# Optimization experiments

Measured on AMD Instinct MI355X. Metric: run time of the kernel, lower is better.

The kernel has to match this reference:

```python
import jax, jax.numpy as jnp
import numpy as np

N, E, IN_DIM, HID, HEADS = 50000, 400000, 128, 64, 4
NEG_SLOPE, LN_EPS = 0.2, 1e-5


def setup_inputs() -> dict:
    key = jax.random.key(0)
    ks = jax.random.split(key, 12)
    x = jax.random.normal(ks[0], (N, IN_DIM), dtype=jnp.float32)
    edge_index = jax.random.randint(ks[1], (2, E), 0, N, dtype=jnp.int64)
    s = 1.0 / np.sqrt(HID)
    return {
        "x": x,
        "edge_index": edge_index,
        "W_gcn": jax.random.normal(ks[2], (IN_DIM, HID), dtype=jnp.float32) / np.sqrt(IN_DIM),
        "b_gcn": jnp.zeros((HID,), dtype=jnp.float32),
        "W_gat": jax.random.normal(ks[3], (HID, HEADS * HID), dtype=jnp.float32) * s,
        "att_src": jax.random.normal(ks[4], (HEADS, HID), dtype=jnp.float32) * s,
        "att_dst": jax.random.normal(ks[5], (HEADS, HID), dtype=jnp.float32) * s,
        "b_gat": jnp.zeros((HID,), dtype=jnp.float32),
        "W_patch": jax.random.normal(ks[6], (HID, HID), dtype=jnp.float32) * s,
        "b_patch": jnp.zeros((HID,), dtype=jnp.float32),
        "gamma": jnp.ones((HID,), dtype=jnp.float32),
        "beta": jnp.zeros((HID,), dtype=jnp.float32),
    }


def _forward(x, edge_index, W_gcn, b_gcn, W_gat, att_src, att_dst, b_gat,
             W_patch, b_patch, gamma, beta):
    n = x.shape[0]
    loop = jnp.arange(n, dtype=edge_index.dtype)
    src = jnp.concatenate([edge_index[0], loop])  # self-loops appended (PyG default)
    dst = jnp.concatenate([edge_index[1], loop])

    # ---- GCNConv: symmetric degree normalization + scatter-add ----
    deg = jax.ops.segment_sum(jnp.ones_like(dst, dtype=jnp.float32), dst, num_segments=n)
    dinv = jnp.where(deg > 0, jax.lax.rsqrt(deg), 0.0)
    norm = dinv[src] * dinv[dst]  # [E+N]
    xw = x @ W_gcn  # [N,HID]
    h1 = jax.ops.segment_sum(xw[src] * norm[:, None], dst, num_segments=n) + b_gcn
    h1 = jax.nn.relu(h1)

    # ---- GATConv (heads=4, concat=False -> mean over heads) ----
    z = (h1 @ W_gat).reshape(n, HEADS, HID)  # [N,H,C]
    a_s = jnp.einsum('nhc,hc->nh', z, att_src)  # [N,H]
    a_d = jnp.einsum('nhc,hc->nh', z, att_dst)
    e = jax.nn.leaky_relu(a_s[src] + a_d[dst], negative_slope=NEG_SLOPE)  # [E+N,H]
    # segment-softmax over incoming edges per destination node
    m = jax.ops.segment_max(e, dst, num_segments=n)  # [N,H]
    ex = jnp.exp(e - m[dst])
    denom = jax.ops.segment_sum(ex, dst, num_segments=n)
    alpha = ex / denom[dst]  # [E+N,H]
    agg = jax.ops.segment_sum(z[src] * alpha[:, :, None], dst, num_segments=n)  # [N,H,C]
    h2 = jax.nn.relu(agg.mean(axis=1) + b_gat)

    # ---- residual fusion + LayerNorm (dropout is identity in eval) ----
    h_patch = h1 @ W_patch + b_patch
    h = h1 + h2 + h_patch
    mu = h.mean(axis=-1, keepdims=True)
    var = h.var(axis=-1, keepdims=True)
    return (h - mu) * jax.lax.rsqrt(var + LN_EPS) * gamma + beta


def reference(x, edge_index, W_gcn, b_gcn, W_gat, att_src, att_dst, b_gat,
              W_patch, b_patch, gamma, beta):
    return _forward(x, edge_index, W_gcn, b_gcn, W_gat, att_src, att_dst, b_gat,
                    W_patch, b_patch, gamma, beta)
```

## Files before the change

### kernel.cpp

```cpp
#include <hip/hip_runtime.h>
#include <math.h>

#define IN_DIM 128
#define HID 64
#define HEADS 4
#define NEG_SLOPE 0.2f
#define LN_EPS 1e-5f
#define XK 320

typedef short bf16x8 __attribute__((ext_vector_type(8)));
typedef float f32x4  __attribute__((ext_vector_type(4)));

__device__ inline unsigned short f2bf(float f) {
    unsigned u = __float_as_uint(f);
    u += 0x7fffu + ((u >> 16) & 1u);
    return (unsigned short)(u >> 16);
}
__device__ inline float bf2f(unsigned short s) {
    return __uint_as_float(((unsigned)s) << 16);
}
__device__ inline float leaky(float v) { return v > 0.0f ? v : NEG_SLOPE * v; }

__global__ void k_detect_zero(const unsigned long long* ei, int count, int n,
                              int* flag, int* hist) {
    int i = blockIdx.x * blockDim.x + threadIdx.x;
    if (i < n) hist[i] = 0;
    if (blockIdx.x == 0) {
        __shared__ int s_bad;
        if (threadIdx.x == 0) s_bad = 0;
        __syncthreads();
        int lim = count < 4096 ? count : 4096;
        int bad = 0;
        for (int k = threadIdx.x; k < lim; k += 256)
            if (ei[k] >= (unsigned long long)n) bad = 1;
        if (bad) s_bad = 1;
        __syncthreads();
        if (threadIdx.x == 0) *flag = s_bad ? 0 : 1;
    }
}

__global__ void k_wprep(const float* __restrict__ Wg, const float* __restrict__ Wp,
                        const float* __restrict__ Wgcn,
                        unsigned short* __restrict__ Wt_post,
                        unsigned short* __restrict__ Wt_xw) {
    int p = blockIdx.x * 256 + threadIdx.x;
    if (p < 2560) {
        int c = p & 63, kg = p >> 6;
        bf16x8 v;
#pragma unroll
        for (int j = 0; j < 8; j++) {
            int k = kg * 8 + j;
            float f;
            if (k < 256) f = 0.25f * Wg[(size_t)(k & 63) * 256 + (k >> 6) * 64 + c];
            else         f = Wp[(size_t)(k - 256) * 64 + c];
            v[j] = (short)f2bf(f);
        }
        *(bf16x8*)(&Wt_post[(size_t)p * 8]) = v;
    } else if (p < 2560 + 1024) {
        int q = p - 2560;
        int c = q & 63, kg = q >> 6;
        bf16x8 v;
#pragma unroll
        for (int j = 0; j < 8; j++)
            v[j] = (short)f2bf(Wgcn[(size_t)(kg * 8 + j) * 64 + c]);
        *(bf16x8*)(&Wt_xw[(size_t)q * 8]) = v;
    }
}

__global__ void k_remap_hist(const void* ei, int E, const int* flag,
                             int* edges32, int* hist) {
    int i = blockIdx.x * blockDim.x + threadIdx.x;
    if (i >= 2 * E) return;
    int is64 = *flag;
    int v;
    if (is64) v = (int)((const long long*)ei)[i];
    else      v = ((const int*)ei)[i];
    edges32[i] = v;
    if (i >= E) atomicAdd(&hist[v], 1);
}

__global__ __launch_bounds__(256) void k_scan1(const int* __restrict__ hist,
                                               int* __restrict__ tmp,
                                               int* __restrict__ partial, int n) {
    __shared__ int s[256];
    int t = threadIdx.x, i = blockIdx.x * 256 + t;
    int v = (i < n) ? hist[i] : 0;
    s[t] = v;
    __syncthreads();
    for (int off = 1; off < 256; off <<= 1) {
        int x = (t >= off) ? s[t - off] : 0;
        __syncthreads();
        s[t] += x;
        __syncthreads();
    }
    tmp[i] = s[t] - v;
    if (t == 255) partial[blockIdx.x] = s[255];
}

__global__ __launch_bounds__(256) void k_scan2_prep(int* partial, int nb,
                                                    const float* __restrict__ Wg,
                                                    const float* __restrict__ att_s,
                                                    const float* __restrict__ att_d,
                                                    float* __restrict__ w_s,
                                                    float* __restrict__ w_d) {
    __shared__ int s[256];
    int t = threadIdx.x;
    int v = (t < nb) ? partial[t] : 0;
    s[t] = v;
    __syncthreads();
    for (int off = 1; off < 256; off <<= 1) {
        int x = (t >= off) ? s[t - off] : 0;
        __syncthreads();
        s[t] += x;
        __syncthreads();
    }
    if (t < nb) partial[t] = s[t] - v;
    int h = t >> 6, k = t & 63;
    float ss = 0.0f, sd = 0.0f;
    for (int c = 0; c < HID; c++) {
        float w = Wg[(size_t)k * (HEADS * HID) + h * HID + c];
        ss += w * att_s[h * HID + c];
        sd += w * att_d[h * HID + c];
    }
    w_s[h * HID + k] = ss;
    w_d[h * HID + k] = sd;
}

__global__ void k_scan3(const int* __restrict__ tmp, const int* __restrict__ partial,
                        const int* __restrict__ hist, int* __restrict__ row_ptr,
                        int* __restrict__ cursor, float* __restrict__ dinv, int n) {
    int i = blockIdx.x * blockDim.x + threadIdx.x;
    if (i >= n) return;
    int v = tmp[i] + partial[i >> 8];
    row_ptr[i] = v;
    cursor[i] = v;
    dinv[i] = rsqrtf((float)(hist[i] + 1));
}

__global__ void k_scatter(const int* __restrict__ src, const int* __restrict__ dst,
                          int* __restrict__ cursor, int* __restrict__ col,
                          int* __restrict__ col_d, int E) {
    int i = blockIdx.x * blockDim.x + threadIdx.x;
    if (i >= E) return;
    int d = dst[i];
    int pos = atomicAdd(&cursor[d], 1);
    col[pos] = src[i];
    col_d[pos] = d;
}

__global__ __launch_bounds__(256) void k_xw(const float* __restrict__ x,
                                            const unsigned short* __restrict__ Wt_g,
                                            const float* __restrict__ dinv,
                                            unsigned short* __restrict__ xws, int n) {
    __shared__ unsigned short Wt[16 * 64 * 8];
    int t = threadIdx.x;
    for (int idx = t; idx < 1024; idx += 256)
        *(bf16x8*)(&Wt[idx * 8]) = *(const bf16x8*)(&Wt_g[(size_t)idx * 8]);
    __syncthreads();

    int lane = t & 63;
    int li = lane & 15, quad = lane >> 4;
    int w = t >> 6;
    int r0 = blockIdx.x * 64 + w * 16;
    int rload = r0 + li; if (rload > n - 1) rload = n - 1;

    f32x4 acc[4];
#pragma unroll
    for (int i = 0; i < 4; i++) acc[i] = (f32x4){0.f, 0.f, 0.f, 0.f};

    const float* xp = x + (size_t)rload * IN_DIM + quad * 8;
#pragma unroll
    for (int ks = 0; ks < 4; ks++) {
        float4 p0 = *(const float4*)(xp + ks * 32);
        float4 p1 = *(const float4*)(xp + ks * 32 + 4);
        bf16x8 a;
        a[0] = (short)f2bf(p0.x); a[1] = (short)f2bf(p0.y);
        a[2] = (short)f2bf(p0.z); a[3] = (short)f2bf(p0.w);
        a[4] = (short)f2bf(p1.x); a[5] = (short)f2bf(p1.y);
        a[6] = (short)f2bf(p1.z); a[7] = (short)f2bf(p1.w);
        int kg = ks * 4 + quad;
#pragma unroll
        for (int tt = 0; tt < 4; tt++) {
            bf16x8 bfr = *(const bf16x8*)(&Wt[((kg * 64) + tt * 16 + li) * 8]);
            acc[tt] = __builtin_amdgcn_mfma_f32_16x16x32_bf16(a, bfr, acc[tt], 0, 0, 0);
        }
    }
#pragma unroll
    for (int reg = 0; reg < 4; reg++) {
        int r = r0 + quad * 4 + reg;
        if (r >= n) continue;
        float dv = dinv[r];
#pragma unroll
        for (int tt = 0; tt < 4; tt++) {
            xws[(size_t)r * HID + tt * 16 + li] = f2bf(acc[tt][reg] * dv);
        }
    }
}

__global__ __launch_bounds__(256) void k_gcn(const int* __restrict__ col,
                                             const int* __restrict__ row_ptr,
                                             const int* __restrict__ hist,
                                             const float* __restrict__ dinv,
                                             const unsigned short* __restrict__ xws,
                                             const float* __restrict__ b,
                                             const float* __restrict__ w_s,
                                             const float* __restrict__ w_d,
                                             float* __restrict__ h1f,
                                             unsigned short* __restrict__ h1b,
                                             unsigned short* __restrict__ X,
                                             float4* __restrict__ a_s,
                                             float4* __restrict__ a_d, int n) {
    int t = threadIdx.x, c = t & 63;
    int d = blockIdx.x * 4 + (t >> 6);
    if (d >= n) return;
    int start = row_ptr[d], cnt = hist[d];
    float acc = bf2f(xws[(size_t)d * HID + c]);
    int k = 0;
    for (; k + 3 < cnt; k += 4) {
        int s0 = col[start + k],     s1 = col[start + k + 1];
        int s2 = col[start + k + 2], s3 = col[start + k + 3];
        float v0 = bf2f(xws[(size_t)s0 * HID + c]);
        float v1 = bf2f(xws[(size_t)s1 * HID + c]);
        float v2 = bf2f(xws[(size_t)s2 * HID + c]);
        float v3 = bf2f(xws[(size_t)s3 * HID + c]);
        acc += (v0 + v1) + (v2 + v3);
    }
    for (; k < cnt; k++) acc += bf2f(xws[(size_t)col[start + k] * HID + c]);
    float h1c = fmaxf(acc * dinv[d] + b[c], 0.0f);
    h1f[(size_t)d * HID + c] = h1c;
    unsigned short hb = f2bf(h1c);
    h1b[(size_t)d * HID + c] = hb;
    X[(size_t)d * XK + 256 + c] = hb;
    float vs0 = h1c * w_s[c],       vs1 = h1c * w_s[64 + c];
    float vs2 = h1c * w_s[128 + c], vs3 = h1c * w_s[192 + c];
    float vd0 = h1c * w_d[c],       vd1 = h1c * w_d[64 + c];
    float vd2 = h1c * w_d[128 + c], vd3 = h1c * w_d[192 + c];
    for (int o = 32; o > 0; o >>= 1) {
        vs0 += __shfl_xor(vs0, o, 64); vs1 += __shfl_xor(vs1, o, 64);
        vs2 += __shfl_xor(vs2, o, 64); vs3 += __shfl_xor(vs3, o, 64);
        vd0 += __shfl_xor(vd0, o, 64); vd1 += __shfl_xor(vd1, o, 64);
        vd2 += __shfl_xor(vd2, o, 64); vd3 += __shfl_xor(vd3, o, 64);
    }
    if (c == 0) {
        a_s[d] = make_float4(vs0, vs1, vs2, vs3);
        a_d[d] = make_float4(vd0, vd1, vd2, vd3);
    }
}

__global__ void k_ew(const int* __restrict__ col, const int* __restrict__ col_d,
                     const float4* __restrict__ a_s, const float4* __restrict__ a_d,
                     float4* __restrict__ wbuf, int E) {
    int i = blockIdx.x * blockDim.x + threadIdx.x;
    if (i >= E) return;
    int s = col[i], d = col_d[i];
    float4 as = a_s[s], ad = a_d[d];
    float4 r;
    r.x = __expf(leaky(as.x + ad.x));
    r.y = __expf(leaky(as.y + ad.y));
    r.z = __expf(leaky(as.z + ad.z));
    r.w = __expf(leaky(as.w + ad.w));
    wbuf[i] = r;
}

__global__ __launch_bounds__(256) void k_attn(const int* __restrict__ col,
                                              const int* __restrict__ row_ptr,
                                              const int* __restrict__ hist,
                                              const float4* __restrict__ a_s,
                                              const float4* __restrict__ a_d,
                                              const float4* __restrict__ wbuf,
                                              const unsigned short* __restrict__ h1b,
                                              unsigned short* __restrict__ X, int n) {
    int t = threadIdx.x, c = t & 63;
    int d = blockIdx.x * 4 + (t >> 6);
    if (d >= n) return;
    float4 ad = a_d[d];
    float4 asd = a_s[d];
    float w0 = __expf(leaky(asd.x + ad.x));
    float w1 = __expf(leaky(asd.y + ad.y));
    float w2 = __expf(leaky(asd.z + ad.z));
    float w3 = __expf(leaky(asd.w + ad.w));
    float hs = bf2f(h1b[(size_t)d * HID + c]);
    float A0 = w0 * hs, A1 = w1 * hs, A2 = w2 * hs, A3 = w3 * hs;
    float l0 = w0, l1 = w1, l2 = w2, l3 = w3;
    int start = row_ptr[d], cnt = hist[d];
    int k = 0;
    for (; k + 3 < cnt; k += 4) {
        int s0 = col[start + k],     s1 = col[start + k + 1];
        int s2 = col[start + k + 2], s3 = col[start + k + 3];
        float4 e0 = wbuf[start + k],     e1 = wbuf[start + k + 1];
        float4 e2 = wbuf[start + k + 2], e3 = wbuf[start + k + 3];
        float hv0 = bf2f(h1b[(size_t)s0 * HID + c]);
        float hv1 = bf2f(h1b[(size_t)s1 * HID + c]);
        float hv2 = bf2f(h1b[(size_t)s2 * HID + c]);
        float hv3 = bf2f(h1b[(size_t)s3 * HID + c]);
        A0 += e0.x * hv0 + e1.x * hv1 + e2.x * hv2 + e3.x * hv3;
        A1 += e0.y * hv0 + e1.y * hv1 + e2.y * hv2 + e3.y * hv3;
        A2 += e0.z * hv0 + e1.z * hv1 + e2.z * hv2 + e3.z * hv3;
        A3 += e0.w * hv0 + e1.w * hv1 + e2.w * hv2 + e3.w * hv3;
        l0 += (e0.x + e1.x) + (e2.x + e3.x);
        l1 += (e0.y + e1.y) + (e2.y + e3.y);
        l2 += (e0.z + e1.z) + (e2.z + e3.z);
        l3 += (e0.w + e1.w) + (e2.w + e3.w);
    }
    for (; k < cnt; k++) {
        int s0 = col[start + k];
        float4 e0 = wbuf[start + k];
        float hv0 = bf2f(h1b[(size_t)s0 * HID + c]);
        A0 += e0.x * hv0; l0 += e0.x;
        A1 += e0.y * hv0; l1 += e0.y;
        A2 += e0.z * hv0; l2 += e0.z;
        A3 += e0.w * hv0; l3 += e0.w;
    }
    size_t base = (size_t)d * XK;
    X[base + c]       = f2bf(A0 / l0);
    X[base + 64 + c]  = f2bf(A1 / l1);
    X[base + 128 + c] = f2bf(A2 / l2);
    X[base + 192 + c] = f2bf(A3 / l3);
}

__global__ __launch_bounds__(256) void k_post(const unsigned short* __restrict__ Wt_g,
                                              const unsigned short* __restrict__ X,
                                              const float* __restrict__ h1f,
                                              const float* __restrict__ bp,
                                              const float* __restrict__ bg,
                                              const float* __restrict__ gamma,
                                              const float* __restrict__ beta,
                                              float* __restrict__ out, int n) {
    __shared__ unsigned short Wt[2560 * 8];
    int t = threadIdx.x;
    for (int idx = t; idx < 2560; idx += 256)
        *(bf16x8*)(&Wt[idx * 8]) = *(const bf16x8*)(&Wt_g[(size_t)idx * 8]);
    __syncthreads();

    int lane = t & 63;
    int li = lane & 15, quad = lane >> 4;
    int w = t >> 6;
    int rbase = blockIdx.x * 128 + w * 32;

    f32x4 acc_a[2][4], acc_h[2][4];
#pragma unroll
    for (int rt = 0; rt < 2; rt++)
#pragma unroll
        for (int i = 0; i < 4; i++) {
            acc_a[rt][i] = (f32x4){0.f, 0.f, 0.f, 0.f};
            acc_h[rt][i] = (f32x4){0.f, 0.f, 0.f, 0.f};
        }
#pragma unroll
    for (int ks = 0; ks < 10; ks++) {
        int kg = ks * 4 + quad;
        bf16x8 b0 = *(const bf16x8*)(&Wt[((kg * 64) + 0 * 16 + li) * 8]);
        bf16x8 b1 = *(const bf16x8*)(&Wt[((kg * 64) + 1 * 16 + li) * 8]);
        bf16x8 b2 = *(const bf16x8*)(&Wt[((kg * 64) + 2 * 16 + li) * 8]);
        bf16x8 b3 = *(const bf16x8*)(&Wt[((kg * 64) + 3 * 16 + li) * 8]);
#pragma unroll
        for (int rt = 0; rt < 2; rt++) {
            bf16x8 a = *(const bf16x8*)(X + (size_t)(rbase + rt * 16 + li) * XK
                                          + quad * 8 + ks * 32);
            if (ks < 8) {
                acc_a[rt][0] = __builtin_amdgcn_mfma_f32_16x16x32_bf16(a, b0, acc_a[rt][0], 0, 0, 0);
                acc_a[rt][1] = __builtin_amdgcn_mfma_f32_16x16x32_bf16(a, b1, acc_a[rt][1], 0, 0, 0);
                acc_a[rt][2] = __builtin_amdgcn_mfma_f32_16x16x32_bf16(a, b2, acc_a[rt][2], 0, 0, 0);
                acc_a[rt][3] = __builtin_amdgcn_mfma_f32_16x16x32_bf16(a, b3, acc_a[rt][3], 0, 0, 0);
            } else {
                acc_h[rt][0] = __builtin_amdgcn_mfma_f32_16x16x32_bf16(a, b0, acc_h[rt][0], 0, 0, 0);
                acc_h[rt][1] = __builtin_amdgcn_mfma_f32_16x16x32_bf16(a, b1, acc_h[rt][1], 0, 0, 0);
                acc_h[rt][2] = __builtin_amdgcn_mfma_f32_16x16x32_bf16(a, b2, acc_h[rt][2], 0, 0, 0);
                acc_h[rt][3] = __builtin_amdgcn_mfma_f32_16x16x32_bf16(a, b3, acc_h[rt][3], 0, 0, 0);
            }
        }
    }
    float bgv[4], bpv[4], gv[4], btv[4];
#pragma unroll
    for (int tt = 0; tt < 4; tt++) {
        int c = tt * 16 + li;
        bgv[tt] = bg[c]; bpv[tt] = bp[c]; gv[tt] = gamma[c]; btv[tt] = beta[c];
    }
#pragma unroll
    for (int rt = 0; rt < 2; rt++) {
#pragma unroll
        for (int reg = 0; reg < 4; reg++) {
            int r = rbase + rt * 16 + quad * 4 + reg;
            bool ok = (r < n);
            float hv[4];
            float s1 = 0.0f, s2 = 0.0f;
#pragma unroll
            for (int tt = 0; tt < 4; tt++) {
                int c = tt * 16 + li;
                float h1c = ok ? h1f[(size_t)r * HID + c] : 0.0f;
                float h2 = fmaxf(acc_a[rt][tt][reg] + bgv[tt], 0.0f);
                float h = h1c + h2 + acc_h[rt][tt][reg] + bpv[tt];
                hv[tt] = h;
                s1 += h; s2 += h * h;
            }
            for (int o = 8; o > 0; o >>= 1) {
                s1 += __shfl_xor(s1, o, 64);
                s2 += __shfl_xor(s2, o, 64);
            }
            float mu = s1 * (1.0f / 64.0f);
            float var = s2 * (1.0f / 64.0f) - mu * mu;
            float rs = rsqrtf(var + LN_EPS);
            if (ok) {
#pragma unroll
                for (int tt = 0; tt < 4; tt++) {
                    int c = tt * 16 + li;
                    out[(size_t)r * HID + c] = (hv[tt] - mu) * rs * gv[tt] + btv[tt];
                }
            }
        }
    }
}

extern "C" void kernel_launch(void* const* d_in, const int* in_sizes, int n_in,
                              void* d_out, int out_size, void* d_ws, size_t ws_size,
                              hipStream_t stream) {
    int n = in_sizes[0] / IN_DIM;
    int E = in_sizes[1] / 2;

    const float* x     = (const float*)d_in[0];
    const void*  ei    = d_in[1];
    const float* W_gcn = (const float*)d_in[2];
    const float* b_gcn = (const float*)d_in[3];
    const float* W_gat = (const float*)d_in[4];
    const float* att_s = (const float*)d_in[5];
    const float* att_d = (const float*)d_in[6];
    const float* b_gat = (const float*)d_in[7];
    const float* W_p   = (const float*)d_in[8];
    const float* b_p   = (const float*)d_in[9];
    const float* gamma = (const float*)d_in[10];
    const float* beta  = (const float*)d_in[11];

    int n_pad  = ((n + 255) / 256) * 256;
    int nscan  = n_pad / 256;
    int n128   = ((n + 127) / 128) * 128;

    float* ws = (float*)d_ws;
    size_t off = 0;
    int*   flag    = (int*)(ws + off);  off += 4;
    int*   edges   = (int*)(ws + off);  off += (size_t)2 * E;
    int*   hist    = (int*)(ws + off);  off += n;
    int*   row_ptr = (int*)(ws + off);  off += n;
    int*   cursor  = (int*)(ws + off);  off += n;
    int*   tmp     = (int*)(ws + off);  off += n_pad;
    int*   partial = (int*)(ws + off);  off += 256;
    int*   colv    = (int*)(ws + off);  off += E;
    int*   col_d   = (int*)(ws + off);  off += E;
    float* dinv    = ws + off;          off += n;
    float* w_s     = ws + off;          off += HEADS * HID;
    float* w_d     = ws + off;          off += HEADS * HID;
    off = (off + 3) & ~(size_t)3;
    unsigned short* Wt_post = (unsigned short*)(ws + off); off += 2560 * 8 / 2;
    unsigned short* Wt_xw   = (unsigned short*)(ws + off); off += 1024 * 8 / 2;
    unsigned short* xws = (unsigned short*)(ws + off); off += (size_t)n * HID / 2;
    float* h1f     = ws + off;          off += (size_t)n * HID;
    off = (off + 3) & ~(size_t)3;
    unsigned short* h1b = (unsigned short*)(ws + off); off += (size_t)n * HID / 2;
    off = (off + 3) & ~(size_t)3;
    float4* a_sv   = (float4*)(ws + off); off += (size_t)n * 4;
    float4* a_dv   = (float4*)(ws + off); off += (size_t)n * 4;
    off = (off + 3) & ~(size_t)3;
    float4* wbuf   = (float4*)(ws + off); off += (size_t)E * 4;
    unsigned short* X = (unsigned short*)(ws + off); off += (size_t)n128 * XK / 2;

    const int* src = edges;
    const int* dst = edges + E;

    k_detect_zero<<<(n + 255) / 256, 256, 0, stream>>>(
        (const unsigned long long*)ei, E, n, flag, hist);
    k_wprep<<<14, 256, 0, stream>>>(W_gat, W_p, W_gcn, Wt_post, Wt_xw);
    k_remap_hist<<<(2 * E + 255) / 256, 256, 0, stream>>>(ei, E, flag, edges, hist);

    k_scan1<<<nscan, 256, 0, stream>>>(hist, tmp, partial, n);
    k_scan2_prep<<<1, 256, 0, stream>>>(partial, nscan, W_gat, att_s, att_d, w_s, w_d);
    k_scan3<<<nscan, 256, 0, stream>>>(tmp, partial, hist, row_ptr, cursor, dinv, n);
    k_scatter<<<(E + 255) / 256, 256, 0, stream>>>(src, dst, cursor, colv, col_d, E);

    k_xw<<<(n + 63) / 64, 256, 0, stream>>>(x, Wt_xw, dinv, xws, n);

    k_gcn<<<(n + 3) / 4, 256, 0, stream>>>(colv, row_ptr, hist, dinv, xws, b_gcn,
                                           w_s, w_d, h1f, h1b, X, a_sv, a_dv, n);

    k_ew<<<(E + 255) / 256, 256, 0, stream>>>(colv, col_d, a_sv, a_dv, wbuf, E);

    k_attn<<<(n + 3) / 4, 256, 0, stream>>>(colv, row_ptr, hist, a_sv, a_dv,
                                            wbuf, h1b, X, n);

    k_post<<<(n + 127) / 128, 256, 0, stream>>>(Wt_post, X, h1f, b_p, b_gat,
                                                gamma, beta, (float*)d_out, n);
}
```

Baseline: 244.5 us.

## Merge init/scatter/xw kernels, drop edge remap buffer and fp32 h1 copy

```diff
diff --git a/kernel.cpp b/kernel.cpp
--- a/kernel.cpp
+++ b/kernel.cpp
@@ -6,7 +6,6 @@
 #define HEADS 4
 #define NEG_SLOPE 0.2f
 #define LN_EPS 1e-5f
-#define XK 320
 
 typedef short bf16x8 __attribute__((ext_vector_type(8)));
 typedef float f32x4  __attribute__((ext_vector_type(4)));
@@ -21,62 +20,62 @@
 }
 __device__ inline float leaky(float v) { return v > 0.0f ? v : NEG_SLOPE * v; }
 
-__global__ void k_detect_zero(const unsigned long long* ei, int count, int n,
-                              int* flag, int* hist) {
+__global__ void k_init_all(const unsigned long long* ei, int E, int n,
+                           int* flag, int* hist,
+                           const float* __restrict__ Wg, const float* __restrict__ Wp,
+                           const float* __restrict__ Wgcn,
+                           unsigned short* __restrict__ Wt_post,
+                           unsigned short* __restrict__ Wt_xw) {
+    int nzb = (n + 255) >> 8;
+    if ((int)blockIdx.x < nzb) {
+        int i = blockIdx.x * 256 + threadIdx.x;
+        if (i < n) hist[i] = 0;
+        if (blockIdx.x == 0) {
+            __shared__ int s_bad;
+            if (threadIdx.x == 0) s_bad = 0;
+            __syncthreads();
+            int lim = E < 4096 ? E : 4096;
+            int bad = 0;
+            for (int k = threadIdx.x; k < lim; k += 256)
+                if (ei[k] >= (unsigned long long)n) bad = 1;
+            if (bad) s_bad = 1;
+            __syncthreads();
+            if (threadIdx.x == 0) *flag = s_bad ? 0 : 1;
+        }
+    } else {
+        int p = (blockIdx.x - nzb) * 256 + threadIdx.x;
+        if (p < 2560) {
+            int c = p & 63, kg = p >> 6;
+            bf16x8 v;
+#pragma unroll
+            for (int j = 0; j < 8; j++) {
+                int k = kg * 8 + j;
+                float f;
+                if (k < 256) f = 0.25f * Wg[(size_t)(k & 63) * 256 + (k >> 6) * 64 + c];
+                else         f = Wp[(size_t)(k - 256) * 64 + c];
+                v[j] = (short)f2bf(f);
+            }
+            *(bf16x8*)(&Wt_post[(size_t)p * 8]) = v;
+        } else if (p < 2560 + 1024) {
+            int q = p - 2560;
+            int c = q & 63, kg = q >> 6;
+            bf16x8 v;
+#pragma unroll
+            for (int j = 0; j < 8; j++)
+                v[j] = (short)f2bf(Wgcn[(size_t)(kg * 8 + j) * 64 + c]);
+            *(bf16x8*)(&Wt_xw[(size_t)q * 8]) = v;
+        }
+    }
+}
+
+__global__ void k_hist(const void* ei, int E, const int* flag, int* hist) {
     int i = blockIdx.x * blockDim.x + threadIdx.x;
-    if (i < n) hist[i] = 0;
-    if (blockIdx.x == 0) {
-        __shared__ int s_bad;
-        if (threadIdx.x == 0) s_bad = 0;
-        __syncthreads();
-        int lim = count < 4096 ? count : 4096;
-        int bad = 0;
-        for (int k = threadIdx.x; k < lim; k += 256)
-            if (ei[k] >= (unsigned long long)n) bad = 1;
-        if (bad) s_bad = 1;
-        __syncthreads();
-        if (threadIdx.x == 0) *flag = s_bad ? 0 : 1;
-    }
-}
-
-__global__ void k_wprep(const float* __restrict__ Wg, const float* __restrict__ Wp,
-                        const float* __restrict__ Wgcn,
-                        unsigned short* __restrict__ Wt_post,
-                        unsigned short* __restrict__ Wt_xw) {
-    int p = blockIdx.x * 256 + threadIdx.x;
-    if (p < 2560) {
-        int c = p & 63, kg = p >> 6;
-        bf16x8 v;
-#pragma unroll
-        for (int j = 0; j < 8; j++) {
-            int k = kg * 8 + j;
-            float f;
-            if (k < 256) f = 0.25f * Wg[(size_t)(k & 63) * 256 + (k >> 6) * 64 + c];
-            else         f = Wp[(size_t)(k - 256) * 64 + c];
-            v[j] = (short)f2bf(f);
-        }
-        *(bf16x8*)(&Wt_post[(size_t)p * 8]) = v;
-    } else if (p < 2560 + 1024) {
-        int q = p - 2560;
-        int c = q & 63, kg = q >> 6;
-        bf16x8 v;
-#pragma unroll
-        for (int j = 0; j < 8; j++)
-            v[j] = (short)f2bf(Wgcn[(size_t)(kg * 8 + j) * 64 + c]);
-        *(bf16x8*)(&Wt_xw[(size_t)q * 8]) = v;
-    }
-}
-
-__global__ void k_remap_hist(const void* ei, int E, const int* flag,
-                             int* edges32, int* hist) {
-    int i = blockIdx.x * blockDim.x + threadIdx.x;
-    if (i >= 2 * E) return;
+    if (i >= E) return;
     int is64 = *flag;
-    int v;
-    if (is64) v = (int)((const long long*)ei)[i];
-    else      v = ((const int*)ei)[i];
-    edges32[i] = v;
-    if (i >= E) atomicAdd(&hist[v], 1);
+    int d;
+    if (is64) d = (int)((const long long*)ei)[E + i];
+    else      d = ((const int*)ei)[E + i];
+    atomicAdd(&hist[d], 1);
 }
 
 __global__ __launch_bounds__(256) void k_scan1(const int* __restrict__ hist,
@@ -137,62 +136,66 @@
     dinv[i] = rsqrtf((float)(hist[i] + 1));
 }
 
-__global__ void k_scatter(const int* __restrict__ src, const int* __restrict__ dst,
-                          int* __restrict__ cursor, int* __restrict__ col,
-                          int* __restrict__ col_d, int E) {
-    int i = blockIdx.x * blockDim.x + threadIdx.x;
-    if (i >= E) return;
-    int d = dst[i];
-    int pos = atomicAdd(&cursor[d], 1);
-    col[pos] = src[i];
-    col_d[pos] = d;
-}
-
-__global__ __launch_bounds__(256) void k_xw(const float* __restrict__ x,
-                                            const unsigned short* __restrict__ Wt_g,
-                                            const float* __restrict__ dinv,
-                                            unsigned short* __restrict__ xws, int n) {
+__global__ __launch_bounds__(256) void k_scatter_xw(const void* ei, int E,
+                                                    const int* __restrict__ flag,
+                                                    int* __restrict__ cursor,
+                                                    int* __restrict__ col,
+                                                    int* __restrict__ col_d,
+                                                    const float* __restrict__ x,
+                                                    const unsigned short* __restrict__ Wt_g,
+                                                    const float* __restrict__ dinv,
+                                                    unsigned short* __restrict__ xws, int n) {
     __shared__ unsigned short Wt[16 * 64 * 8];
-    int t = threadIdx.x;
-    for (int idx = t; idx < 1024; idx += 256)
-        *(bf16x8*)(&Wt[idx * 8]) = *(const bf16x8*)(&Wt_g[(size_t)idx * 8]);
-    __syncthreads();
-
-    int lane = t & 63;
-    int li = lane & 15, quad = lane >> 4;
-    int w = t >> 6;
-    int r0 = blockIdx.x * 64 + w * 16;
-    int rload = r0 + li; if (rload > n - 1) rload = n - 1;
-
-    f32x4 acc[4];
-#pragma unroll
-    for (int i = 0; i < 4; i++) acc[i] = (f32x4){0.f, 0.f, 0.f, 0.f};
-
-    const float* xp = x + (size_t)rload * IN_DIM + quad * 8;
-#pragma unroll
-    for (int ks = 0; ks < 4; ks++) {
-        float4 p0 = *(const float4*)(xp + ks * 32);
-        float4 p1 = *(const float4*)(xp + ks * 32 + 4);
-        bf16x8 a;
-        a[0] = (short)f2bf(p0.x); a[1] = (short)f2bf(p0.y);
-        a[2] = (short)f2bf(p0.z); a[3] = (short)f2bf(p0.w);
-        a[4] = (short)f2bf(p1.x); a[5] = (short)f2bf(p1.y);
-        a[6] = (short)f2bf(p1.z); a[7] = (short)f2bf(p1.w);
-        int kg = ks * 4 + quad;
-#pragma unroll
-        for (int tt = 0; tt < 4; tt++) {
-            bf16x8 bfr = *(const bf16x8*)(&Wt[((kg * 64) + tt * 16 + li) * 8]);
-            acc[tt] = __builtin_amdgcn_mfma_f32_16x16x32_bf16(a, bfr, acc[tt], 0, 0, 0);
-        }
-    }
-#pragma unroll
-    for (int reg = 0; reg < 4; reg++) {
-        int r = r0 + quad * 4 + reg;
-        if (r >= n) continue;
-        float dv = dinv[r];
-#pragma unroll
-        for (int tt = 0; tt < 4; tt++) {
-            xws[(size_t)r * HID + tt * 16 + li] = f2bf(acc[tt][reg] * dv);
+    int nsb = (E + 255) >> 8;
+    if ((int)blockIdx.x < nsb) {
+        int i = blockIdx.x * 256 + threadIdx.x;
+        if (i >= E) return;
+        int is64 = *flag;
+        int s, d;
+        if (is64) { s = (int)((const long long*)ei)[i]; d = (int)((const long long*)ei)[E + i]; }
+        else      { s = ((const int*)ei)[i];            d = ((const int*)ei)[E + i]; }
+        int pos = atomicAdd(&cursor[d], 1);
+        col[pos] = s;
+        col_d[pos] = d;
+    } else {
+        int bx = blockIdx.x - nsb;
+        int t = threadIdx.x;
+        for (int idx = t; idx < 1024; idx += 256)
+            *(bf16x8*)(&Wt[idx * 8]) = *(const bf16x8*)(&Wt_g[(size_t)idx * 8]);
+        __syncthreads();
+        int lane = t & 63;
+        int li = lane & 15, quad = lane >> 4;
+        int w = t >> 6;
+        int r0 = bx * 64 + w * 16;
+        int rload = r0 + li; if (rload > n - 1) rload = n - 1;
+        f32x4 acc[4];
+#pragma unroll
+        for (int i = 0; i < 4; i++) acc[i] = (f32x4){0.f, 0.f, 0.f, 0.f};
+        const float* xp = x + (size_t)rload * IN_DIM + quad * 8;
+#pragma unroll
+        for (int ks = 0; ks < 4; ks++) {
+            float4 p0 = *(const float4*)(xp + ks * 32);
+            float4 p1 = *(const float4*)(xp + ks * 32 + 4);
+            bf16x8 a;
+            a[0] = (short)f2bf(p0.x); a[1] = (short)f2bf(p0.y);
+            a[2] = (short)f2bf(p0.z); a[3] = (short)f2bf(p0.w);
+            a[4] = (short)f2bf(p1.x); a[5] = (short)f2bf(p1.y);
+            a[6] = (short)f2bf(p1.z); a[7] = (short)f2bf(p1.w);
+            int kg = ks * 4 + quad;
+#pragma unroll
+            for (int tt = 0; tt < 4; tt++) {
+                bf16x8 bfr = *(const bf16x8*)(&Wt[((kg * 64) + tt * 16 + li) * 8]);
+                acc[tt] = __builtin_amdgcn_mfma_f32_16x16x32_bf16(a, bfr, acc[tt], 0, 0, 0);
+            }
+        }
+#pragma unroll
+        for (int reg = 0; reg < 4; reg++) {
+            int r = r0 + quad * 4 + reg;
+            if (r >= n) continue;
+            float dv = dinv[r];
+#pragma unroll
+            for (int tt = 0; tt < 4; tt++)
+                xws[(size_t)r * HID + tt * 16 + li] = f2bf(acc[tt][reg] * dv);
         }
     }
 }
@@ -205,9 +208,7 @@
                                              const float* __restrict__ b,
                                              const float* __restrict__ w_s,
                                              const float* __restrict__ w_d,
-                                             float* __restrict__ h1f,
                                              unsigned short* __restrict__ h1b,
-                                             unsigned short* __restrict__ X,
                                              float4* __restrict__ a_s,
                                              float4* __restrict__ a_d, int n) {
     int t = threadIdx.x, c = t & 63;
@@ -216,21 +217,24 @@
     int start = row_ptr[d], cnt = hist[d];
     float acc = bf2f(xws[(size_t)d * HID + c]);
     int k = 0;
-    for (; k + 3 < cnt; k += 4) {
+    for (; k + 7 < cnt; k += 8) {
         int s0 = col[start + k],     s1 = col[start + k + 1];
         int s2 = col[start + k + 2], s3 = col[start + k + 3];
+        int s4 = col[start + k + 4], s5 = col[start + k + 5];
+        int s6 = col[start + k + 6], s7 = col[start + k + 7];
         float v0 = bf2f(xws[(size_t)s0 * HID + c]);
         float v1 = bf2f(xws[(size_t)s1 * HID + c]);
         float v2 = bf2f(xws[(size_t)s2 * HID + c]);
         float v3 = bf2f(xws[(size_t)s3 * HID + c]);
-        acc += (v0 + v1) + (v2 + v3);
+        float v4 = bf2f(xws[(size_t)s4 * HID + c]);
+        float v5 = bf2f(xws[(size_t)s5 * HID + c]);
+        float v6 = bf2f(xws[(size_t)s6 * HID + c]);
+        float v7 = bf2f(xws[(size_t)s7 * HID + c]);
+        acc += ((v0 + v1) + (v2 + v3)) + ((v4 + v5) + (v6 + v7));
     }
     for (; k < cnt; k++) acc += bf2f(xws[(size_t)col[start + k] * HID + c]);
     float h1c = fmaxf(acc * dinv[d] + b[c], 0.0f);
-    h1f[(size_t)d * HID + c] = h1c;
-    unsigned short hb = f2bf(h1c);
-    h1b[(size_t)d * HID + c] = hb;
-    X[(size_t)d * XK + 256 + c] = hb;
+    h1b[(size_t)d * HID + c] = f2bf(h1c);
     float vs0 = h1c * w_s[c],       vs1 = h1c * w_s[64 + c];
     float vs2 = h1c * w_s[128 + c], vs3 = h1c * w_s[192 + c];
     float vd0 = h1c * w_d[c],       vd1 = h1c * w_d[64 + c];
@@ -284,23 +288,18 @@
     float l0 = w0, l1 = w1, l2 = w2, l3 = w3;
     int start = row_ptr[d], cnt = hist[d];
     int k = 0;
-    for (; k + 3 < cnt; k += 4) {
-        int s0 = col[start + k],     s1 = col[start + k + 1];
-        int s2 = col[start + k + 2], s3 = col[start + k + 3];
-        float4 e0 = wbuf[start + k],     e1 = wbuf[start + k + 1];
-        float4 e2 = wbuf[start + k + 2], e3 = wbuf[start + k + 3];
-        float hv0 = bf2f(h1b[(size_t)s0 * HID + c]);
-        float hv1 = bf2f(h1b[(size_t)s1 * HID + c]);
-        float hv2 = bf2f(h1b[(size_t)s2 * HID + c]);
-        float hv3 = bf2f(h1b[(size_t)s3 * HID + c]);
-        A0 += e0.x * hv0 + e1.x * hv1 + e2.x * hv2 + e3.x * hv3;
-        A1 += e0.y * hv0 + e1.y * hv1 + e2.y * hv2 + e3.y * hv3;
-        A2 += e0.z * hv0 + e1.z * hv1 + e2.z * hv2 + e3.z * hv3;
-        A3 += e0.w * hv0 + e1.w * hv1 + e2.w * hv2 + e3.w * hv3;
-        l0 += (e0.x + e1.x) + (e2.x + e3.x);
-        l1 += (e0.y + e1.y) + (e2.y + e3.y);
-        l2 += (e0.z + e1.z) + (e2.z + e3.z);
-        l3 += (e0.w + e1.w) + (e2.w + e3.w);
+    for (; k + 7 < cnt; k += 8) {
+#pragma unroll
+        for (int j = 0; j < 8; j += 2) {
+            int sa = col[start + k + j], sb = col[start + k + j + 1];
+            float4 ea = wbuf[start + k + j], eb = wbuf[start + k + j + 1];
+            float ha = bf2f(h1b[(size_t)sa * HID + c]);
+            float hb = bf2f(h1b[(size_t)sb * HID + c]);
+            A0 += ea.x * ha + eb.x * hb; l0 += ea.x + eb.x;
+            A1 += ea.y * ha + eb.y * hb; l1 += ea.y + eb.y;
+            A2 += ea.z * ha + eb.z * hb; l2 += ea.z + eb.z;
+            A3 += ea.w * ha + eb.w * hb; l3 += ea.w + eb.w;
+        }
     }
     for (; k < cnt; k++) {
         int s0 = col[start + k];
@@ -311,7 +310,7 @@
         A2 += e0.z * hv0; l2 += e0.z;
         A3 += e0.w * hv0; l3 += e0.w;
     }
-    size_t base = (size_t)d * XK;
+    size_t base = (size_t)d * 256;
     X[base + c]       = f2bf(A0 / l0);
     X[base + 64 + c]  = f2bf(A1 / l1);
     X[base + 128 + c] = f2bf(A2 / l2);
@@ -320,7 +319,7 @@
 
 __global__ __launch_bounds__(256) void k_post(const unsigned short* __restrict__ Wt_g,
                                               const unsigned short* __restrict__ X,
-                                              const float* __restrict__ h1f,
+                                              const unsigned short* __restrict__ h1b,
                                               const float* __restrict__ bp,
                                               const float* __restrict__ bg,
                                               const float* __restrict__ gamma,
@@ -354,8 +353,12 @@
         bf16x8 b3 = *(const bf16x8*)(&Wt[((kg * 64) + 3 * 16 + li) * 8]);
 #pragma unroll
         for (int rt = 0; rt < 2; rt++) {
-            bf16x8 a = *(const bf16x8*)(X + (size_t)(rbase + rt * 16 + li) * XK
-                                          + quad * 8 + ks * 32);
+            int row = rbase + rt * 16 + li;
+            bf16x8 a;
+            if (ks < 8)
+                a = *(const bf16x8*)(X + (size_t)row * 256 + quad * 8 + ks * 32);
+            else
+                a = *(const bf16x8*)(h1b + (size_t)row * HID + quad * 8 + (ks - 8) * 32);
             if (ks < 8) {
                 acc_a[rt][0] = __builtin_amdgcn_mfma_f32_16x16x32_bf16(a, b0, acc_a[rt][0], 0, 0, 0);
                 acc_a[rt][1] = __builtin_amdgcn_mfma_f32_16x16x32_bf16(a, b1, acc_a[rt][1], 0, 0, 0);
@@ -386,7 +389,7 @@
 #pragma unroll
             for (int tt = 0; tt < 4; tt++) {
                 int c = tt * 16 + li;
-                float h1c = ok ? h1f[(size_t)r * HID + c] : 0.0f;
+                float h1c = ok ? bf2f(h1b[(size_t)r * HID + c]) : 0.0f;
                 float h2 = fmaxf(acc_a[rt][tt][reg] + bgv[tt], 0.0f);
                 float h = h1c + h2 + acc_h[rt][tt][reg] + bpv[tt];
                 hv[tt] = h;
@@ -432,11 +435,12 @@
     int n_pad  = ((n + 255) / 256) * 256;
     int nscan  = n_pad / 256;
     int n128   = ((n + 127) / 128) * 128;
+    int nzb    = (n + 255) / 256;
+    int nsb    = (E + 255) / 256;
 
     float* ws = (float*)d_ws;
     size_t off = 0;
     int*   flag    = (int*)(ws + off);  off += 4;
-    int*   edges   = (int*)(ws + off);  off += (size_t)2 * E;
     int*   hist    = (int*)(ws + off);  off += n;
     int*   row_ptr = (int*)(ws + off);  off += n;
     int*   cursor  = (int*)(ws + off);  off += n;
@@ -451,39 +455,36 @@
     unsigned short* Wt_post = (unsigned short*)(ws + off); off += 2560 * 8 / 2;
     unsigned short* Wt_xw   = (unsigned short*)(ws + off); off += 1024 * 8 / 2;
     unsigned short* xws = (unsigned short*)(ws + off); off += (size_t)n * HID / 2;
-    float* h1f     = ws + off;          off += (size_t)n * HID;
     off = (off + 3) & ~(size_t)3;
-    unsigned short* h1b = (unsigned short*)(ws + off); off += (size_t)n * HID / 2;
+    unsigned short* h1b = (unsigned short*)(ws + off); off += (size_t)n128 * HID / 2;
     off = (off + 3) & ~(size_t)3;
     float4* a_sv   = (float4*)(ws + off); off += (size_t)n * 4;
     float4* a_dv   = (float4*)(ws + off); off += (size_t)n * 4;
     off = (off + 3) & ~(size_t)3;
     float4* wbuf   = (float4*)(ws + off); off += (size_t)E * 4;
-    unsigned short* X = (unsigned short*)(ws + off); off += (size_t)n128 * XK / 2;
-
-    const int* src = edges;
-    const int* dst = edges + E;
-
-    k_detect_zero<<<(n + 255) / 256, 256, 0, stream>>>(
-        (const unsigned long long*)ei, E, n, flag, hist);
-    k_wprep<<<14, 256, 0, stream>>>(W_gat, W_p, W_gcn, Wt_post, Wt_xw);
-    k_remap_hist<<<(2 * E + 255) / 256, 256, 0, stream>>>(ei, E, flag, edges, hist);
+    unsigned short* X = (unsigned short*)(ws + off); off += (size_t)n128 * 256 / 2;
+
+    k_init_all<<<nzb + 14, 256, 0, stream>>>((const unsigned long long*)ei, E, n,
+                                             flag, hist, W_gat, W_p, W_gcn,
+                                             Wt_post, Wt_xw);
+    k_hist<<<nsb, 256, 0, stream>>>(ei, E, flag, hist);
 
     k_scan1<<<nscan, 256, 0, stream>>>(hist, tmp, partial, n);
     k_scan2_prep<<<1, 256, 0, stream>>>(partial, nscan, W_gat, att_s, att_d, w_s, w_d);
     k_scan3<<<nscan, 256, 0, stream>>>(tmp, partial, hist, row_ptr, cursor, dinv, n);
-    k_scatter<<<(E + 255) / 256, 256, 0, stream>>>(src, dst, cursor, colv, col_d, E);
-
-    k_xw<<<(n + 63) / 64, 256, 0, stream>>>(x, Wt_xw, dinv, xws, n);
+
+    k_scatter_xw<<<nsb + (n + 63) / 64, 256, 0, stream>>>(ei, E, flag, cursor,
+                                                          colv, col_d, x, Wt_xw,
+                                                          dinv, xws, n);
 
     k_gcn<<<(n + 3) / 4, 256, 0, stream>>>(colv, row_ptr, hist, dinv, xws, b_gcn,
-                                           w_s, w_d, h1f, h1b, X, a_sv, a_dv, n);
+                                           w_s, w_d, h1b, a_sv, a_dv, n);
 
     k_ew<<<(E + 255) / 256, 256, 0, stream>>>(colv, col_d, a_sv, a_dv, wbuf, E);
 
     k_attn<<<(n + 3) / 4, 256, 0, stream>>>(colv, row_ptr, hist, a_sv, a_dv,
                                             wbuf, h1b, X, n);
 
-    k_post<<<(n + 127) / 128, 256, 0, stream>>>(Wt_post, X, h1f, b_p, b_gat,
+    k_post<<<(n + 127) / 128, 256, 0, stream>>>(Wt_post, X, h1b, b_p, b_gat,
                                                 gamma, beta, (float*)d_out, n);
 }
```

After: 255.2 us. +4.3%, slower.
